# Optimization experiments

Measured on AMD Instinct MI355X. Metric: run time of the kernel, lower is better.

The kernel has to match this reference:

```python
import jax, jax.numpy as jnp
import numpy as np
import math

B, N, D, H, L = 2, 512, 256, 8, 3
EPS = 1e-4


def setup_inputs() -> dict:
    key = jax.random.key(0)
    ks = jax.random.split(key, 16)
    # valid boxes (x1, y1, x2, y2) with positive width/height
    xy = jax.random.uniform(ks[0], (B, N, 2), dtype=jnp.float32) * 800.0
    wh = jax.random.uniform(ks[1], (B, N, 2), dtype=jnp.float32) * 200.0 + 1.0
    boxes = jnp.concatenate([xy, xy + wh], axis=-1)
    features = jax.random.normal(ks[2], (B, N, D), dtype=jnp.float32)
    mask = jnp.ones((B, N, N), dtype=jnp.int32)
    s = 1.0 / math.sqrt(D)
    Wq = jax.random.normal(ks[3], (L, D, D), dtype=jnp.float32) * s
    Wk = jax.random.normal(ks[4], (L, D, D), dtype=jnp.float32) * s
    Wv = jax.random.normal(ks[5], (L, D, D), dtype=jnp.float32) * s
    Wo = jax.random.normal(ks[6], (L, D, D), dtype=jnp.float32) * s
    Wg = jax.random.normal(ks[7], (L, D, H), dtype=jnp.float32) * s
    bq = jnp.zeros((L, D), jnp.float32)
    bk = jnp.zeros((L, D), jnp.float32)
    bv = jnp.zeros((L, D), jnp.float32)
    bo = jnp.zeros((L, D), jnp.float32)
    bg = jnp.zeros((L, H), jnp.float32)
    feat_range = jnp.arange(D // 8, dtype=jnp.float32)
    div_mat = jnp.power(1000.0, (8.0 / D) * feat_range) / 100.0
    return dict(boxes=boxes, features=features, mask=mask,
                Wq=Wq, bq=bq, Wk=Wk, bk=bk, Wv=Wv, bv=bv, Wo=Wo, bo=bo,
                Wg=Wg, bg=bg, div_mat=div_mat)


def _position_embedding(boxes, div_mat):
    # relative geometry between all box pairs (q == k == boxes)
    cx = (boxes[..., 0] + boxes[..., 2]) / 2
    cy = (boxes[..., 1] + boxes[..., 3]) / 2
    w = jnp.maximum(boxes[..., 2] - boxes[..., 0], EPS)
    h = jnp.maximum(boxes[..., 3] - boxes[..., 1], EPS)
    rel_x = jnp.log(jnp.abs(cx[:, None, :] - cx[:, :, None]) / w[:, None, :] + EPS)
    rel_y = jnp.log(jnp.abs(cy[:, None, :] - cy[:, :, None]) / h[:, None, :] + EPS)
    rel_w = jnp.log(w[:, :, None] / w[:, None, :] + EPS)
    rel_h = jnp.log(h[:, :, None] / h[:, None, :] + EPS)
    rel = jnp.stack([rel_x, rel_y, rel_w, rel_h], axis=-1)  # (B,N,N,4)
    pm = rel[..., None] / div_mat                            # (B,N,N,4,D/8)
    emb = jnp.concatenate([jnp.sin(pm), jnp.cos(pm)], axis=-1)  # (B,N,N,4,D/4)
    return emb.reshape(*emb.shape[:3], -1)                   # (B,N,N,D)


def reference(boxes, features, mask, Wq, bq, Wk, bk, Wv, bv, Wo, bo, Wg, bg, div_mat):
    emb = _position_embedding(boxes, div_mat)  # (B,N,N,D)
    dh = D // H
    inv_sqrt_dk = 1.0 / math.sqrt(dh)
    mask_b = (mask[:, None, :, :] == 0)  # (B,1,N,N)
    x = features

    def heads(t):  # (B,N,D) -> (B,H,N,dh)
        return t.reshape(B, N, H, dh).transpose(0, 2, 1, 3)

    for l in range(L):
        q = jax.nn.relu(x @ Wq[l] + bq[l])
        k = jax.nn.relu(x @ Wk[l] + bk[l])
        v = jax.nn.relu(x @ Wv[l] + bv[l])
        qh, kh, vh = heads(q), heads(k), heads(v)
        geo = jax.nn.relu(emb @ Wg[l] + bg[l])           # (B,N,N,H)
        geo = geo.transpose(0, 3, 1, 2)                   # (B,H,N,N)
        scores = jnp.einsum('bhqd,bhkd->bhqk', qh, kh) * inv_sqrt_dk
        scores = scores + jnp.log(geo + 1e-6)
        scores = jnp.where(mask_b, -1e9, scores)
        atten = jax.nn.softmax(scores, axis=-1)
        y = jnp.einsum('bhqk,bhkd->bhqd', atten, vh)      # (B,H,N,dh)
        y = y.transpose(0, 2, 1, 3).reshape(B, N, D)
        y = jax.nn.relu(y @ Wo[l] + bo[l])
        x = x + y
    return x
```

## Files before the change

kernel.cpp:

```cpp
#include <hip/hip_runtime.h>
#include <hip/hip_fp16.h>

#define BB 2
#define NNq 512
#define DDm 256
#define HHh 8
#define DHh 32
#define LLn 3

static constexpr float EPSF   = 1e-4f;
static constexpr float INV2PI = 0.15915494309189535f;
static constexpr float SCALE  = 0.17677669529663687f;

#if __has_builtin(__builtin_amdgcn_fractf)
#define FRACTF(x) __builtin_amdgcn_fractf(x)
#else
#define FRACTF(x) ((x) - floorf(x))
#endif
#if __has_builtin(__builtin_amdgcn_sinf)
#define SINR(x) __builtin_amdgcn_sinf(x)
#define COSR(x) __builtin_amdgcn_cosf(x)
#else
#define SINR(x) __sinf((x) * 6.2831853071795865f)
#define COSR(x) __cosf((x) * 6.2831853071795865f)
#endif

typedef _Float16 f16x8 __attribute__((ext_vector_type(8)));
typedef _Float16 f16x4 __attribute__((ext_vector_type(4)));
typedef _Float16 f16x2 __attribute__((ext_vector_type(2)));
typedef float    f32x4 __attribute__((ext_vector_type(4)));

__device__ inline f16x2 pk2(float a, float b) {
#if __has_builtin(__builtin_amdgcn_cvt_pkrtz)
    return __builtin_bit_cast(f16x2, __builtin_amdgcn_cvt_pkrtz(a, b));
#else
    f16x2 r; r[0] = (_Float16)a; r[1] = (_Float16)b; return r;
#endif
}
union U16x8 { f16x8 v; f16x2 h[4]; };

__global__ __launch_bounds__(256) void k_wcvt(const float* __restrict__ Wq,
        const float* __restrict__ Wk, const float* __restrict__ Wv,
        const float* __restrict__ Wo, _Float16* __restrict__ WT,
        const float* __restrict__ Wg, _Float16* __restrict__ WgTg) {
    __shared__ _Float16 t[64][72];
    const int tid = threadIdx.x;
    const int mat = blockIdx.z;
    if (mat == 12) {
        if (blockIdx.x == 0 && blockIdx.y == 0) {
            for (int idx = tid; idx < 32 * 256; idx += 256) {
                int n = idx >> 8, k = idx & 255;
                float w = (n < 24) ? Wg[(size_t)(n >> 3) * 2048 + (size_t)k * 8 + (n & 7)] : 0.f;
                WgTg[n * 256 + (k ^ ((n & 7) << 3))] = (_Float16)w;
            }
        }
        return;
    }
    const int l = mat >> 2, op = mat & 3;
    const float* W = (op == 0 ? Wq : op == 1 ? Wk : op == 2 ? Wv : Wo)
                     + (size_t)l * 65536;
    const int k0 = blockIdx.x * 64, n0 = blockIdx.y * 64;
    for (int u = tid; u < 64 * 16; u += 256) {
        int k = u >> 4, n4 = (u & 15) * 4;
        float4 w4 = *reinterpret_cast<const float4*>(&W[(size_t)(k0 + k) * 256 + n0 + n4]);
        t[n4 + 0][k] = (_Float16)w4.x; t[n4 + 1][k] = (_Float16)w4.y;
        t[n4 + 2][k] = (_Float16)w4.z; t[n4 + 3][k] = (_Float16)w4.w;
    }
    __syncthreads();
    for (int u = tid; u < 64 * 8; u += 256) {
        int n = u >> 3, kc = (u & 7) * 8;
        *reinterpret_cast<f16x8*>(&WT[((size_t)mat * 256 + n0 + n) * 256 + k0 + kc]) =
            *reinterpret_cast<const f16x8*>(&t[n][kc]);
    }
}

__global__ __launch_bounds__(256, 4) void k_geo(const float* __restrict__ boxes,
                                                const _Float16* __restrict__ WgTg,
                                                const float* __restrict__ bg,
                                                const float* __restrict__ divm,
                                                const int* __restrict__ maskp,
                                                __half* __restrict__ G) {
    __shared__ __half obuf[4][24][68];

    const int tid  = threadIdx.x;
    const int lane = tid & 63;
    const int wid  = tid >> 6;
    const int ln15 = lane & 15;
    const int kgrp = lane >> 4;

    float invd[8];
    {
        const float4* dv4 = reinterpret_cast<const float4*>(divm);
        float4 da = dv4[kgrp * 2], db = dv4[kgrp * 2 + 1];
        invd[0] = INV2PI / da.x; invd[1] = INV2PI / da.y;
        invd[2] = INV2PI / da.z; invd[3] = INV2PI / da.w;
        invd[4] = INV2PI / db.x; invd[5] = INV2PI / db.y;
        invd[6] = INV2PI / db.z; invd[7] = INV2PI / db.w;
    }
    const int n0 = ln15;
    const int n1 = 16 + ln15;
    const float bg0 = bg[n0];
    const float bg1 = (n1 < 24) ? bg[n1] : 0.f;

    const int mask  = (ln15 & 7) << 3;
    const int flip5 = mask & 32;
    const int kb    = (kgrp << 3) ^ (mask & 24);
    const int base0 = n0 * 256 + kb;
    const int base1 = n1 * 256 + kb;

    f16x8 bS0[4], bC0[4], bS1[4], bC1[4];
#pragma unroll
    for (int kc2 = 0; kc2 < 4; ++kc2) {
        const int koffS = ((2 * kc2) * 32) ^ flip5;
        const int koffC = ((2 * kc2 + 1) * 32) ^ flip5;
        bS0[kc2] = *reinterpret_cast<const f16x8*>(&WgTg[base0 + koffS]);
        bC0[kc2] = *reinterpret_cast<const f16x8*>(&WgTg[base0 + koffC]);
        bS1[kc2] = *reinterpret_cast<const f16x8*>(&WgTg[base1 + koffS]);
        bC1[kc2] = *reinterpret_cast<const f16x8*>(&WgTg[base1 + koffC]);
    }

    const float4* boxes4 = reinterpret_cast<const float4*>(boxes);
    const size_t plane = (size_t)NNq * NNq;

    const int base4 = (blockIdx.x * 4 + wid) * 4;
#pragma unroll
    for (int it = 0; it < 4; ++it) {
        const int slab = base4 + it;
        const int p0 = slab << 4;
        const int b  = p0 >> 18;
        const int rem = p0 & (NNq * NNq - 1);
        const int i  = rem >> 9;
        const int j0 = rem & (NNq - 1);

        float4 Bi = boxes4[b * NNq + i];
        float4 Bj = boxes4[b * NNq + j0 + ln15];
        float cxi = 0.5f * (Bi.x + Bi.z), cyi = 0.5f * (Bi.y + Bi.w);
        float wi  = fmaxf(Bi.z - Bi.x, EPSF), hi = fmaxf(Bi.w - Bi.y, EPSF);
        float cxj = 0.5f * (Bj.x + Bj.z), cyj = 0.5f * (Bj.y + Bj.w);
        float wj  = fmaxf(Bj.z - Bj.x, EPSF), hj = fmaxf(Bj.w - Bj.y, EPSF);
        float rel[4];
        rel[0] = __logf(fabsf(cxj - cxi) / wj + EPSF);
        rel[1] = __logf(fabsf(cyj - cyi) / hj + EPSF);
        rel[2] = __logf(wi / wj + EPSF);
        rel[3] = __logf(hi / hj + EPSF);

        f32x4 acc0 = {0.f, 0.f, 0.f, 0.f};
        f32x4 acc1 = {0.f, 0.f, 0.f, 0.f};

#pragma unroll
        for (int kc2 = 0; kc2 < 4; ++kc2) {
            const float rc = rel[kc2];
            U16x8 afs, afc;
#pragma unroll
            for (int jj = 0; jj < 4; ++jj) {
                float rv0 = FRACTF(rc * invd[2 * jj]);
                float rv1 = FRACTF(rc * invd[2 * jj + 1]);
                afs.h[jj] = pk2(SINR(rv0), SINR(rv1));
                afc.h[jj] = pk2(COSR(rv0), COSR(rv1));
            }
            acc0 = __builtin_amdgcn_mfma_f32_16x16x32_f16(afs.v, bS0[kc2], acc0, 0, 0, 0);
            acc0 = __builtin_amdgcn_mfma_f32_16x16x32_f16(afc.v, bC0[kc2], acc0, 0, 0, 0);
            acc1 = __builtin_amdgcn_mfma_f32_16x16x32_f16(afs.v, bS1[kc2], acc1, 0, 0, 0);
            acc1 = __builtin_amdgcn_mfma_f32_16x16x32_f16(afc.v, bC1[kc2], acc1, 0, 0, 0);
        }

#pragma unroll
        for (int r = 0; r < 4; ++r) {
            const int m = it * 16 + (kgrp << 2) + r;
            float g0 = fmaxf(acc0[r] + bg0, 0.f);
            obuf[wid][n0][m] = __float2half(g0);
            if (n1 < 24) {
                float g1 = fmaxf(acc1[r] + bg1, 0.f);
                obuf[wid][n1][m] = __float2half(g1);
            }
        }
    }
    __syncthreads();

    const int b_  = base4 >> 14;
    const int i_  = (base4 >> 5) & (NNq - 1);
    const int j0b = (base4 & 31) << 4;
    const int mv  = maskp[((size_t)b_ * NNq + i_) * NNq + j0b + lane];
    size_t obase = (size_t)b_ * plane + (size_t)i_ * NNq + j0b + lane;
#pragma unroll
    for (int t = 0; t < 24; ++t) {
        float g = __half2float(obuf[wid][t][lane]);
        float v = (mv != 0) ? (g + 1e-6f) : 0.0f;
        G[obase + (size_t)t * (BB * plane)] = __float2half(v);
    }
}

#define LDP 264
__global__ __launch_bounds__(256) void k_gemm_qkv(const float* __restrict__ A,
        const _Float16* __restrict__ WT0, const _Float16* __restrict__ WT1,
        const _Float16* __restrict__ WT2,
        const float* __restrict__ b0, const float* __restrict__ b1, const float* __restrict__ b2,
        _Float16* __restrict__ C0, _Float16* __restrict__ C1, _Float16* __restrict__ C2) {
    const _Float16* WTz = (blockIdx.z == 0) ? WT0 : (blockIdx.z == 1) ? WT1 : WT2;
    const float*    bia = (blockIdx.z == 0) ? b0 : (blockIdx.z == 1) ? b1 : b2;
    _Float16*       C   = (blockIdx.z == 0) ? C0 : (blockIdx.z == 1) ? C1 : C2;

    __shared__ _Float16 As[32 * LDP];
    __shared__ _Float16 Ws[64 * LDP];

    const int tid = threadIdx.x;
    const int m0 = blockIdx.x * 32, n0 = blockIdx.y * 64;

    for (int u = tid; u < 32 * 64; u += 256) {
        int m = u >> 6, k4 = (u & 63) * 4;
        float4 av = *reinterpret_cast<const float4*>(&A[(size_t)(m0 + m) * 256 + k4]);
        f16x4 hv = {(_Float16)av.x, (_Float16)av.y, (_Float16)av.z, (_Float16)av.w};
        *reinterpret_cast<f16x4*>(&As[m * LDP + k4]) = hv;
    }
    for (int u = tid; u < 2048; u += 256) {
        int n = u >> 5, kc = (u & 31) * 8;
        *reinterpret_cast<f16x8*>(&Ws[n * LDP + kc]) =
            *reinterpret_cast<const f16x8*>(&WTz[(size_t)(n0 + n) * 256 + kc]);
    }
    __syncthreads();

    const int lane = tid & 63;
    const int wid  = tid >> 6;
    const int ln15 = lane & 15;
    const int kgrp = lane >> 4;
    const int mw   = (wid & 1) * 16;
    const int nsel = (wid >> 1) * 16;
    const int kfr  = kgrp * 8;

    f32x4 acc[2] = {{0.f,0.f,0.f,0.f},{0.f,0.f,0.f,0.f}};
#pragma unroll
    for (int kc = 0; kc < 8; ++kc) {
        f16x8 af = *reinterpret_cast<const f16x8*>(&As[(mw + ln15) * LDP + kc * 32 + kfr]);
#pragma unroll
        for (int t = 0; t < 2; ++t) {
            f16x8 bf = *reinterpret_cast<const f16x8*>(
                &Ws[(nsel + t * 32 + ln15) * LDP + kc * 32 + kfr]);
            acc[t] = __builtin_amdgcn_mfma_f32_16x16x32_f16(af, bf, acc[t], 0, 0, 0);
        }
    }

#pragma unroll
    for (int t = 0; t < 2; ++t) {
        const int col = n0 + nsel + t * 32 + ln15;
        const float bv = bia[col];
#pragma unroll
        for (int r = 0; r < 4; ++r) {
            const int row = m0 + mw + kgrp * 4 + r;
            C[(size_t)row * 256 + col] = (_Float16)fmaxf(acc[t][r] + bv, 0.f);
        }
    }
}

__global__ __launch_bounds__(256) void k_gemm_o(const _Float16* __restrict__ A,
        const _Float16* __restrict__ WT0,
        const float* __restrict__ bia,
        float* __restrict__ C, const float* __restrict__ resid) {
    __shared__ _Float16 As[32 * LDP];
    __shared__ _Float16 Ws[64 * LDP];

    const int tid = threadIdx.x;
    const int m0 = blockIdx.x * 32, n0 = blockIdx.y * 64;

    for (int u = tid; u < 1024; u += 256) {
        int m = u >> 5, kc = (u & 31) * 8;
        *reinterpret_cast<f16x8*>(&As[m * LDP + kc]) =
            *reinterpret_cast<const f16x8*>(&A[(size_t)(m0 + m) * 256 + kc]);
    }
    for (int u = tid; u < 2048; u += 256) {
        int n = u >> 5, kc = (u & 31) * 8;
        *reinterpret_cast<f16x8*>(&Ws[n * LDP + kc]) =
            *reinterpret_cast<const f16x8*>(&WT0[(size_t)(n0 + n) * 256 + kc]);
    }
    __syncthreads();

    const int lane = tid & 63;
    const int wid  = tid >> 6;
    const int ln15 = lane & 15;
    const int kgrp = lane >> 4;
    const int mw   = (wid & 1) * 16;
    const int nsel = (wid >> 1) * 16;
    const int kfr  = kgrp * 8;

    f32x4 acc[2] = {{0.f,0.f,0.f,0.f},{0.f,0.f,0.f,0.f}};
#pragma unroll
    for (int kc = 0; kc < 8; ++kc) {
        f16x8 af = *reinterpret_cast<const f16x8*>(&As[(mw + ln15) * LDP + kc * 32 + kfr]);
#pragma unroll
        for (int t = 0; t < 2; ++t) {
            f16x8 bf = *reinterpret_cast<const f16x8*>(
                &Ws[(nsel + t * 32 + ln15) * LDP + kc * 32 + kfr]);
            acc[t] = __builtin_amdgcn_mfma_f32_16x16x32_f16(af, bf, acc[t], 0, 0, 0);
        }
    }

#pragma unroll
    for (int t = 0; t < 2; ++t) {
        const int col = n0 + nsel + t * 32 + ln15;
        const float bv = bia[col];
#pragma unroll
        for (int r = 0; r < 4; ++r) {
            const int row = m0 + mw + kgrp * 4 + r;
            float o = fmaxf(acc[t][r] + bv, 0.f) + resid[(size_t)row * 256 + col];
            C[(size_t)row * 256 + col] = o;
        }
    }
}

__global__ __launch_bounds__(256) void k_attn(const _Float16* __restrict__ q,
                                              const _Float16* __restrict__ kk,
                                              const _Float16* __restrict__ vv,
                                              const __half* __restrict__ G,
                                              _Float16* __restrict__ y, int l) {
    __shared__ _Float16 Kh[512 * 32];
    __shared__ _Float16 VT[32 * 512];
    __shared__ _Float16 Ps[4][16 * 128];

    const int bh = blockIdx.y;
    const int b = bh >> 3, h = bh & 7;
    const int i0t = blockIdx.x * 16;

    const int tid  = threadIdx.x;
    const int lane = tid & 63, wid = tid >> 6;
    const int ln15 = lane & 15, kgrp = lane >> 4;

    for (int u = tid; u < 2048; u += 256) {
        int j = u >> 2, d8 = (u & 3) * 8;
        const size_t src = (size_t)(b * NNq + j) * DDm + h * DHh + d8;
        f16x8 kv = *reinterpret_cast<const f16x8*>(&kk[src]);
        *reinterpret_cast<f16x8*>(reinterpret_cast<char*>(Kh) +
            ((j * 64 + d8 * 2) ^ ((j & 7) << 4))) = kv;
        f16x8 v8 = *reinterpret_cast<const f16x8*>(&vv[src]);
#pragma unroll
        for (int e = 0; e < 8; ++e) {
            int row = d8 + e;
            *reinterpret_cast<_Float16*>(reinterpret_cast<char*>(VT) +
                ((row * 1024 + j * 2) ^ ((row & 7) << 4))) = v8[e];
        }
    }

    f16x8 qf = *reinterpret_cast<const f16x8*>(
        &q[(size_t)(b * NNq + i0t + ln15) * DDm + h * DHh + kgrp * 8]);
    __syncthreads();

    const int jbase = wid * 128;
    const size_t plane = (size_t)NNq * NNq;
    const size_t g_base = (size_t)((l * 8 + h) * BB + b) * plane;

    f32x4 s[8];
#pragma unroll
    for (int t = 0; t < 8; ++t) {
        int j = jbase + t * 16 + ln15;
        f16x8 kf = *reinterpret_cast<const f16x8*>(reinterpret_cast<char*>(Kh) +
            ((j * 64 + kgrp * 16) ^ ((j & 7) << 4)));
        f32x4 z = {0.f, 0.f, 0.f, 0.f};
        s[t] = __builtin_amdgcn_mfma_f32_16x16x32_f16(qf, kf, z, 0, 0, 0);
    }

    float gv[8][4];
#pragma unroll
    for (int t = 0; t < 8; ++t) {
        const size_t jg = jbase + t * 16 + ln15;
#pragma unroll
        for (int r = 0; r < 4; ++r)
            gv[t][r] = __half2float(G[g_base + (size_t)(i0t + kgrp * 4 + r) * NNq + jg]);
    }

    float m_[4], l_[4];
#pragma unroll
    for (int r = 0; r < 4; ++r) {
        float mx = s[0][r];
#pragma unroll
        for (int t = 1; t < 8; ++t) mx = fmaxf(mx, s[t][r]);
        mx *= SCALE;
#pragma unroll
        for (int o = 1; o < 16; o <<= 1) mx = fmaxf(mx, __shfl_xor(mx, o, 64));
        float sum = 0.f;
#pragma unroll
        for (int t = 0; t < 8; ++t) {
            float p = gv[t][r] * __expf(s[t][r] * SCALE - mx);
            s[t][r] = p; sum += p;
        }
#pragma unroll
        for (int o = 1; o < 16; o <<= 1) sum += __shfl_xor(sum, o, 64);
        m_[r] = mx; l_[r] = sum;
    }

    {
        char* psb = reinterpret_cast<char*>(Ps[wid]);
#pragma unroll
        for (int r = 0; r < 4; ++r) {
            const int row = kgrp * 4 + r;
            const int rb = row * 256, sw = (row & 7) << 4;
#pragma unroll
            for (int t = 0; t < 8; ++t) {
                int byte = (rb + (t * 16 + ln15) * 2) ^ sw;
                *reinterpret_cast<_Float16*>(psb + byte) = (_Float16)s[t][r];
            }
        }
    }

    f32x4 oacc[2] = {{0.f,0.f,0.f,0.f},{0.f,0.f,0.f,0.f}};
    {
        char* psb = reinterpret_cast<char*>(Ps[wid]);
#pragma unroll
        for (int kc = 0; kc < 4; ++kc) {
            f16x8 pf = *reinterpret_cast<const f16x8*>(psb +
                ((ln15 * 256 + kc * 64 + kgrp * 16) ^ ((ln15 & 7) << 4)));
#pragma unroll
            for (int dt = 0; dt < 2; ++dt) {
                int d = dt * 16 + ln15;
                f16x8 vf = *reinterpret_cast<const f16x8*>(reinterpret_cast<char*>(VT) +
                    ((d * 1024 + (jbase + kc * 32 + kgrp * 8) * 2) ^ ((d & 7) << 4)));
                oacc[dt] = __builtin_amdgcn_mfma_f32_16x16x32_f16(pf, vf, oacc[dt], 0, 0, 0);
            }
        }
    }

    {
        float* Op = reinterpret_cast<float*>(reinterpret_cast<char*>(Kh) + wid * 8192);
#pragma unroll
        for (int dt = 0; dt < 2; ++dt)
#pragma unroll
            for (int r = 0; r < 4; ++r)
                Op[(kgrp * 4 + r) * 32 + dt * 16 + ln15] = oacc[dt][r];
        if (ln15 == 0) {
#pragma unroll
            for (int r = 0; r < 4; ++r) {
                Op[512 + kgrp * 4 + r] = m_[r];
                Op[528 + kgrp * 4 + r] = l_[r];
            }
        }
    }
    __syncthreads();

    {
        const int i = tid >> 4, d0 = (tid & 15) * 2;
        float mw[4], M = -3.0e38f;
#pragma unroll
        for (int w = 0; w < 4; ++w) {
            mw[w] = reinterpret_cast<float*>(reinterpret_cast<char*>(Kh) + w * 8192)[512 + i];
            M = fmaxf(M, mw[w]);
        }
        float o0 = 0.f, o1 = 0.f, ls = 0.f;
#pragma unroll
        for (int w = 0; w < 4; ++w) {
            float* Op = reinterpret_cast<float*>(reinterpret_cast<char*>(Kh) + w * 8192);
            float sc = __expf(mw[w] - M);
            ls += Op[528 + i] * sc;
            o0 += Op[i * 32 + d0] * sc;
            o1 += Op[i * 32 + d0 + 1] * sc;
        }
        float inv = 1.0f / ls;
        f16x2 ov; ov[0] = (_Float16)(o0 * inv); ov[1] = (_Float16)(o1 * inv);
        *reinterpret_cast<f16x2*>(&y[(size_t)(b * NNq + i0t + i) * DDm + h * DHh + d0]) = ov;
    }
}

extern "C" void kernel_launch(void* const* d_in, const int* in_sizes, int n_in,
                              void* d_out, int out_size, void* d_ws, size_t ws_size,
                              hipStream_t stream) {
    const float* boxes    = (const float*)d_in[0];
    const float* features = (const float*)d_in[1];
    const int*   mask     = (const int*)d_in[2];
    const float* Wq = (const float*)d_in[3];
    const float* bq = (const float*)d_in[4];
    const float* Wk = (const float*)d_in[5];
    const float* bk = (const float*)d_in[6];
    const float* Wv = (const float*)d_in[7];
    const float* bv = (const float*)d_in[8];
    const float* Wo = (const float*)d_in[9];
    const float* bo = (const float*)d_in[10];
    const float* Wg = (const float*)d_in[11];
    const float* bg = (const float*)d_in[12];
    const float* dv = (const float*)d_in[13];

    char* ws = (char*)d_ws;
    __half*    Gb   = (__half*)(ws);
    _Float16*  WT   = (_Float16*)(ws + 25165824);
    _Float16*  WgTg = (_Float16*)(ws + 26738688);
    _Float16*  qb   = (_Float16*)(ws + 26755072);
    _Float16*  kb   = (_Float16*)(ws + 27279360);
    _Float16*  vb   = (_Float16*)(ws + 27803648);
    _Float16*  yb   = (_Float16*)(ws + 28327936);
    float*     x    = (float*)d_out;

    k_wcvt<<<dim3(4, 4, 13), dim3(256), 0, stream>>>(Wq, Wk, Wv, Wo, WT, Wg, WgTg);
    k_geo<<<dim3(2048), dim3(256), 0, stream>>>(boxes, WgTg, bg, dv, mask, Gb);

    for (int l = 0; l < LLn; ++l) {
        const _Float16* WTq = WT + (size_t)(l * 4 + 0) * 65536;
        const _Float16* WTk = WT + (size_t)(l * 4 + 1) * 65536;
        const _Float16* WTv = WT + (size_t)(l * 4 + 2) * 65536;
        const _Float16* WTo = WT + (size_t)(l * 4 + 3) * 65536;
        const float* bq_l = bq + (size_t)l * DDm;
        const float* bk_l = bk + (size_t)l * DDm;
        const float* bv_l = bv + (size_t)l * DDm;
        const float* bo_l = bo + (size_t)l * DDm;
        const float* xin  = (l == 0) ? features : x;

        k_gemm_qkv<<<dim3(32, 4, 3), dim3(256), 0, stream>>>(
            xin, WTq, WTk, WTv, bq_l, bk_l, bv_l, qb, kb, vb);
        k_attn<<<dim3(32, 16), dim3(256), 0, stream>>>(qb, kb, vb, Gb, yb, l);
        k_gemm_o<<<dim3(32, 4), dim3(256), 0, stream>>>(
            yb, WTo, bo_l, x, xin);
    }
}
```

Measured before the change: 101.3 us.

## Fuse layer-0 QKV GEMM into geo kernel and drop LDS staging in GEMMs

Extra blocks are appended to the geometry kernel so it also computes the layer-0 Q/K/V projection, which removes one launch. The QKV and output GEMMs now load fragments straight from global memory instead of staging them in LDS. The output GEMM also writes an fp16 copy of x, so later QKV GEMMs read half-precision input without converting it. The geometry kernel replaces its divisions with hardware reciprocals, which slightly changes precision.

```diff
diff --git a/kernel.cpp b/kernel.cpp
--- a/kernel.cpp
+++ b/kernel.cpp
@@ -23,6 +23,11 @@
 #else
 #define SINR(x) __sinf((x) * 6.2831853071795865f)
 #define COSR(x) __cosf((x) * 6.2831853071795865f)
+#endif
+#if __has_builtin(__builtin_amdgcn_rcpf)
+#define RCPF(x) __builtin_amdgcn_rcpf(x)
+#else
+#define RCPF(x) (1.0f / (x))
 #endif
 
 typedef _Float16 f16x8 __attribute__((ext_vector_type(8)));
@@ -74,12 +79,15 @@
     }
 }
 
-__global__ __launch_bounds__(256, 4) void k_geo(const float* __restrict__ boxes,
-                                                const _Float16* __restrict__ WgTg,
-                                                const float* __restrict__ bg,
-                                                const float* __restrict__ divm,
-                                                const int* __restrict__ maskp,
-                                                __half* __restrict__ G) {
+__global__ __launch_bounds__(256, 4) void k_geo_qkv0(const float* __restrict__ boxes,
+        const _Float16* __restrict__ WgTg, const float* __restrict__ bg,
+        const float* __restrict__ divm, const int* __restrict__ maskp,
+        __half* __restrict__ G,
+        const float* __restrict__ feat, const _Float16* __restrict__ WT,
+        const float* __restrict__ bq, const float* __restrict__ bk,
+        const float* __restrict__ bv,
+        _Float16* __restrict__ qb, _Float16* __restrict__ kb,
+        _Float16* __restrict__ vb) {
     __shared__ __half obuf[4][24][68];
 
     const int tid  = threadIdx.x;
@@ -87,6 +95,49 @@
     const int wid  = tid >> 6;
     const int ln15 = lane & 15;
     const int kgrp = lane >> 4;
+
+    if ((int)blockIdx.x >= 2048) {
+        const int q = blockIdx.x - 2048;
+        const int z = q >> 7;
+        const int rem = q & 127;
+        const int m0 = (rem >> 2) * 32, n0 = (rem & 3) * 64;
+        const _Float16* WTz = WT + (size_t)z * 65536;
+        const float* bia = (z == 0) ? bq : (z == 1) ? bk : bv;
+        _Float16* C = (z == 0) ? qb : (z == 1) ? kb : vb;
+
+        const int mw   = (wid & 1) * 16;
+        const int nsel = (wid >> 1) * 16;
+        const int kfr  = kgrp * 8;
+
+        const float* Arow = feat + (size_t)(m0 + mw + ln15) * 256;
+        const _Float16* W0r = WTz + (size_t)(n0 + nsel + ln15) * 256;
+        const _Float16* W1r = WTz + (size_t)(n0 + nsel + 32 + ln15) * 256;
+
+        f32x4 acc[2] = {{0.f,0.f,0.f,0.f},{0.f,0.f,0.f,0.f}};
+#pragma unroll
+        for (int kc = 0; kc < 8; ++kc) {
+            float4 a0 = *reinterpret_cast<const float4*>(Arow + kc * 32 + kfr);
+            float4 a1 = *reinterpret_cast<const float4*>(Arow + kc * 32 + kfr + 4);
+            U16x8 af;
+            af.h[0] = pk2(a0.x, a0.y); af.h[1] = pk2(a0.z, a0.w);
+            af.h[2] = pk2(a1.x, a1.y); af.h[3] = pk2(a1.z, a1.w);
+            f16x8 b0 = *reinterpret_cast<const f16x8*>(W0r + kc * 32 + kfr);
+            f16x8 b1 = *reinterpret_cast<const f16x8*>(W1r + kc * 32 + kfr);
+            acc[0] = __builtin_amdgcn_mfma_f32_16x16x32_f16(af.v, b0, acc[0], 0, 0, 0);
+            acc[1] = __builtin_amdgcn_mfma_f32_16x16x32_f16(af.v, b1, acc[1], 0, 0, 0);
+        }
+#pragma unroll
+        for (int t = 0; t < 2; ++t) {
+            const int col = n0 + nsel + t * 32 + ln15;
+            const float bv_ = bia[col];
+#pragma unroll
+            for (int r = 0; r < 4; ++r) {
+                const int row = m0 + mw + kgrp * 4 + r;
+                C[(size_t)row * 256 + col] = (_Float16)fmaxf(acc[t][r] + bv_, 0.f);
+            }
+        }
+        return;
+    }
 
     float invd[8];
     {
@@ -104,9 +155,9 @@
 
     const int mask  = (ln15 & 7) << 3;
     const int flip5 = mask & 32;
-    const int kb    = (kgrp << 3) ^ (mask & 24);
-    const int base0 = n0 * 256 + kb;
-    const int base1 = n1 * 256 + kb;
+    const int kb_   = (kgrp << 3) ^ (mask & 24);
+    const int base0 = n0 * 256 + kb_;
+    const int base1 = n1 * 256 + kb_;
 
     f16x8 bS0[4], bC0[4], bS1[4], bC1[4];
 #pragma unroll
@@ -138,11 +189,12 @@
         float wi  = fmaxf(Bi.z - Bi.x, EPSF), hi = fmaxf(Bi.w - Bi.y, EPSF);
         float cxj = 0.5f * (Bj.x + Bj.z), cyj = 0.5f * (Bj.y + Bj.w);
         float wj  = fmaxf(Bj.z - Bj.x, EPSF), hj = fmaxf(Bj.w - Bj.y, EPSF);
+        float rwj = RCPF(wj), rhj = RCPF(hj);
         float rel[4];
-        rel[0] = __logf(fabsf(cxj - cxi) / wj + EPSF);
-        rel[1] = __logf(fabsf(cyj - cyi) / hj + EPSF);
-        rel[2] = __logf(wi / wj + EPSF);
-        rel[3] = __logf(hi / hj + EPSF);
+        rel[0] = __logf(fabsf(cxj - cxi) * rwj + EPSF);
+        rel[1] = __logf(fabsf(cyj - cyi) * rhj + EPSF);
+        rel[2] = __logf(wi * rwj + EPSF);
+        rel[3] = __logf(hi * rhj + EPSF);
 
         f32x4 acc0 = {0.f, 0.f, 0.f, 0.f};
         f32x4 acc1 = {0.f, 0.f, 0.f, 0.f};
@@ -190,8 +242,7 @@
     }
 }
 
-#define LDP 264
-__global__ __launch_bounds__(256) void k_gemm_qkv(const float* __restrict__ A,
+__global__ __launch_bounds__(256) void k_gemm_qkv_h(const _Float16* __restrict__ A,
         const _Float16* __restrict__ WT0, const _Float16* __restrict__ WT1,
         const _Float16* __restrict__ WT2,
         const float* __restrict__ b0, const float* __restrict__ b1, const float* __restrict__ b2,
@@ -200,45 +251,27 @@
     const float*    bia = (blockIdx.z == 0) ? b0 : (blockIdx.z == 1) ? b1 : b2;
     _Float16*       C   = (blockIdx.z == 0) ? C0 : (blockIdx.z == 1) ? C1 : C2;
 
-    __shared__ _Float16 As[32 * LDP];
-    __shared__ _Float16 Ws[64 * LDP];
-
-    const int tid = threadIdx.x;
+    const int tid  = threadIdx.x;
+    const int lane = tid & 63, wid = tid >> 6;
+    const int ln15 = lane & 15, kgrp = lane >> 4;
     const int m0 = blockIdx.x * 32, n0 = blockIdx.y * 64;
-
-    for (int u = tid; u < 32 * 64; u += 256) {
-        int m = u >> 6, k4 = (u & 63) * 4;
-        float4 av = *reinterpret_cast<const float4*>(&A[(size_t)(m0 + m) * 256 + k4]);
-        f16x4 hv = {(_Float16)av.x, (_Float16)av.y, (_Float16)av.z, (_Float16)av.w};
-        *reinterpret_cast<f16x4*>(&As[m * LDP + k4]) = hv;
-    }
-    for (int u = tid; u < 2048; u += 256) {
-        int n = u >> 5, kc = (u & 31) * 8;
-        *reinterpret_cast<f16x8*>(&Ws[n * LDP + kc]) =
-            *reinterpret_cast<const f16x8*>(&WTz[(size_t)(n0 + n) * 256 + kc]);
-    }
-    __syncthreads();
-
-    const int lane = tid & 63;
-    const int wid  = tid >> 6;
-    const int ln15 = lane & 15;
-    const int kgrp = lane >> 4;
     const int mw   = (wid & 1) * 16;
     const int nsel = (wid >> 1) * 16;
     const int kfr  = kgrp * 8;
 
+    const _Float16* Arow = A + (size_t)(m0 + mw + ln15) * 256;
+    const _Float16* W0r  = WTz + (size_t)(n0 + nsel + ln15) * 256;
+    const _Float16* W1r  = WTz + (size_t)(n0 + nsel + 32 + ln15) * 256;
+
     f32x4 acc[2] = {{0.f,0.f,0.f,0.f},{0.f,0.f,0.f,0.f}};
 #pragma unroll
     for (int kc = 0; kc < 8; ++kc) {
-        f16x8 af = *reinterpret_cast<const f16x8*>(&As[(mw + ln15) * LDP + kc * 32 + kfr]);
-#pragma unroll
-        for (int t = 0; t < 2; ++t) {
-            f16x8 bf = *reinterpret_cast<const f16x8*>(
-                &Ws[(nsel + t * 32 + ln15) * LDP + kc * 32 + kfr]);
-            acc[t] = __builtin_amdgcn_mfma_f32_16x16x32_f16(af, bf, acc[t], 0, 0, 0);
-        }
-    }
-
+        f16x8 af = *reinterpret_cast<const f16x8*>(Arow + kc * 32 + kfr);
+        f16x8 b0_ = *reinterpret_cast<const f16x8*>(W0r + kc * 32 + kfr);
+        f16x8 b1_ = *reinterpret_cast<const f16x8*>(W1r + kc * 32 + kfr);
+        acc[0] = __builtin_amdgcn_mfma_f32_16x16x32_f16(af, b0_, acc[0], 0, 0, 0);
+        acc[1] = __builtin_amdgcn_mfma_f32_16x16x32_f16(af, b1_, acc[1], 0, 0, 0);
+    }
 #pragma unroll
     for (int t = 0; t < 2; ++t) {
         const int col = n0 + nsel + t * 32 + ln15;
@@ -252,47 +285,30 @@
 }
 
 __global__ __launch_bounds__(256) void k_gemm_o(const _Float16* __restrict__ A,
-        const _Float16* __restrict__ WT0,
-        const float* __restrict__ bia,
-        float* __restrict__ C, const float* __restrict__ resid) {
-    __shared__ _Float16 As[32 * LDP];
-    __shared__ _Float16 Ws[64 * LDP];
-
-    const int tid = threadIdx.x;
+        const _Float16* __restrict__ WT0, const float* __restrict__ bia,
+        float* __restrict__ C, _Float16* __restrict__ Ch,
+        const float* __restrict__ resid) {
+    const int tid  = threadIdx.x;
+    const int lane = tid & 63, wid = tid >> 6;
+    const int ln15 = lane & 15, kgrp = lane >> 4;
     const int m0 = blockIdx.x * 32, n0 = blockIdx.y * 64;
-
-    for (int u = tid; u < 1024; u += 256) {
-        int m = u >> 5, kc = (u & 31) * 8;
-        *reinterpret_cast<f16x8*>(&As[m * LDP + kc]) =
-            *reinterpret_cast<const f16x8*>(&A[(size_t)(m0 + m) * 256 + kc]);
-    }
-    for (int u = tid; u < 2048; u += 256) {
-        int n = u >> 5, kc = (u & 31) * 8;
-        *reinterpret_cast<f16x8*>(&Ws[n * LDP + kc]) =
-            *reinterpret_cast<const f16x8*>(&WT0[(size_t)(n0 + n) * 256 + kc]);
-    }
-    __syncthreads();
-
-    const int lane = tid & 63;
-    const int wid  = tid >> 6;
-    const int ln15 = lane & 15;
-    const int kgrp = lane >> 4;
     const int mw   = (wid & 1) * 16;
     const int nsel = (wid >> 1) * 16;
     const int kfr  = kgrp * 8;
 
+    const _Float16* Arow = A + (size_t)(m0 + mw + ln15) * 256;
+    const _Float16* W0r  = WT0 + (size_t)(n0 + nsel + ln15) * 256;
+    const _Float16* W1r  = WT0 + (size_t)(n0 + nsel + 32 + ln15) * 256;
+
     f32x4 acc[2] = {{0.f,0.f,0.f,0.f},{0.f,0.f,0.f,0.f}};
 #pragma unroll
     for (int kc = 0; kc < 8; ++kc) {
-        f16x8 af = *reinterpret_cast<const f16x8*>(&As[(mw + ln15) * LDP + kc * 32 + kfr]);
-#pragma unroll
-        for (int t = 0; t < 2; ++t) {
-            f16x8 bf = *reinterpret_cast<const f16x8*>(
-                &Ws[(nsel + t * 32 + ln15) * LDP + kc * 32 + kfr]);
-            acc[t] = __builtin_amdgcn_mfma_f32_16x16x32_f16(af, bf, acc[t], 0, 0, 0);
-        }
-    }
-
+        f16x8 af = *reinterpret_cast<const f16x8*>(Arow + kc * 32 + kfr);
+        f16x8 b0_ = *reinterpret_cast<const f16x8*>(W0r + kc * 32 + kfr);
+        f16x8 b1_ = *reinterpret_cast<const f16x8*>(W1r + kc * 32 + kfr);
+        acc[0] = __builtin_amdgcn_mfma_f32_16x16x32_f16(af, b0_, acc[0], 0, 0, 0);
+        acc[1] = __builtin_amdgcn_mfma_f32_16x16x32_f16(af, b1_, acc[1], 0, 0, 0);
+    }
 #pragma unroll
     for (int t = 0; t < 2; ++t) {
         const int col = n0 + nsel + t * 32 + ln15;
@@ -302,6 +318,7 @@
             const int row = m0 + mw + kgrp * 4 + r;
             float o = fmaxf(acc[t][r] + bv, 0.f) + resid[(size_t)row * 256 + col];
             C[(size_t)row * 256 + col] = o;
+            Ch[(size_t)row * 256 + col] = (_Float16)o;
         }
     }
 }
@@ -482,10 +499,13 @@
     _Float16*  kb   = (_Float16*)(ws + 27279360);
     _Float16*  vb   = (_Float16*)(ws + 27803648);
     _Float16*  yb   = (_Float16*)(ws + 28327936);
+    _Float16*  xh   = (_Float16*)(ws + 28852224);
     float*     x    = (float*)d_out;
 
     k_wcvt<<<dim3(4, 4, 13), dim3(256), 0, stream>>>(Wq, Wk, Wv, Wo, WT, Wg, WgTg);
-    k_geo<<<dim3(2048), dim3(256), 0, stream>>>(boxes, WgTg, bg, dv, mask, Gb);
+    k_geo_qkv0<<<dim3(2432), dim3(256), 0, stream>>>(
+        boxes, WgTg, bg, dv, mask, Gb,
+        features, WT, bq, bk, bv, qb, kb, vb);
 
     for (int l = 0; l < LLn; ++l) {
         const _Float16* WTq = WT + (size_t)(l * 4 + 0) * 65536;
@@ -496,12 +516,18 @@
         const float* bk_l = bk + (size_t)l * DDm;
         const float* bv_l = bv + (size_t)l * DDm;
         const float* bo_l = bo + (size_t)l * DDm;
-        const float* xin  = (l == 0) ? features : x;
-
-        k_gemm_qkv<<<dim3(32, 4, 3), dim3(256), 0, stream>>>(
-            xin, WTq, WTk, WTv, bq_l, bk_l, bv_l, qb, kb, vb);
+
+        if (l > 0) {
+            k_gemm_qkv_h<<<dim3(32, 4, 3), dim3(256), 0, stream>>>(
+                xh, WTq, WTk, WTv, bq_l, bk_l, bv_l, qb, kb, vb);
+        }
         k_attn<<<dim3(32, 16), dim3(256), 0, stream>>>(qb, kb, vb, Gb, yb, l);
-        k_gemm_o<<<dim3(32, 4), dim3(256), 0, stream>>>(
-            yb, WTo, bo_l, x, xin);
-    }
-}
+        if (l == 0) {
+            k_gemm_o<<<dim3(32, 4), dim3(256), 0, stream>>>(
+                yb, WTo, bo_l, x, xh, features);
+        } else {
+            k_gemm_o<<<dim3(32, 4), dim3(256), 0, stream>>>(
+                yb, WTo, bo_l, x, xh, x);
+        }
+    }
+}
```

New measurement: 99.91 us. About the same (-1.4%).
